# Kernel optimization log

Hardware: AMD Instinct MI355X
Metric: run time of the kernel (lower is better)

## Reference

```python
import jax, jax.numpy as jnp
import numpy as np

HEADS = 8
DIM_HEAD = 64
EPS = 1e-5

def chan_norm(x, g, b):
    # LayerNorm over channel dim (axis=1), biased variance
    mean = jnp.mean(x, axis=1, keepdims=True)
    var = jnp.var(x, axis=1, keepdims=True)
    return (x - mean) / jnp.sqrt(var + EPS) * g + b

def l2norm(x):
    n = jnp.sqrt(jnp.sum(x * x, axis=1, keepdims=True))
    return x / jnp.maximum(n, 1e-12)

def fold_heads(x, b):
    # b (h c) H W -> (b h) c H W
    _, hc, H, W = x.shape
    return x.reshape(b, HEADS, DIM_HEAD, H, W).reshape(b * HEADS, DIM_HEAD, H, W)

def setup_inputs() -> dict:
    key = jax.random.key(0)
    ks = jax.random.split(key, 8)
    dim = 256
    inner = HEADS * DIM_HEAD  # 512
    b, Hq, Wq = 8, 96, 96
    Hc, Wc = 64, 64
    s = 1.0 / np.sqrt(dim)
    return {
        "query_source": jax.random.normal(ks[0], (b, dim, Hq, Wq), jnp.float32),
        "context": jax.random.normal(ks[1], (b, dim, Hc, Wc), jnp.float32),
        "qs_g": jnp.ones((1, dim, 1, 1), jnp.float32),
        "qs_b": jnp.zeros((1, dim, 1, 1), jnp.float32),
        "ctx_g": jnp.ones((1, dim, 1, 1), jnp.float32),
        "ctx_b": jnp.zeros((1, dim, 1, 1), jnp.float32),
        "out_g": jnp.ones((1, dim, 1, 1), jnp.float32),
        "out_b": jnp.zeros((1, dim, 1, 1), jnp.float32),
        "w_q": jax.random.normal(ks[2], (inner, dim), jnp.float32) * s,
        "w_kv": jax.random.normal(ks[3], (2 * inner, dim), jnp.float32) * s,
        "w_out": jax.random.normal(ks[4], (dim, inner), jnp.float32) * (1.0 / np.sqrt(inner)),
        "gamma": jnp.full((1,), 0.5, jnp.float32),
    }

def reference(query_source, context, qs_g, qs_b, ctx_g, ctx_b, out_g, out_b, w_q, w_kv, w_out, gamma):
    b, c, Hq, Wq = query_source.shape
    Hc, Wc = context.shape[2], context.shape[3]
    h_top_k = int(Hc ** 0.5)
    w_top_k = int(Wc ** 0.5)

    ctx = chan_norm(context, ctx_g, ctx_b)
    qs = chan_norm(query_source, qs_g, qs_b)

    kv = jnp.einsum('oc,bchw->bohw', w_kv, ctx)  # 1x1 conv, no bias
    k, v = jnp.split(kv, 2, axis=1)
    q = jnp.einsum('oc,bchw->bohw', w_q, qs)

    q = fold_heads(q, b); k = fold_heads(k, b); v = fold_heads(v, b)
    q = l2norm(q); k = l2norm(k)  # cosine-sim attention

    if h_top_k < Hc or w_top_k < Wc:
        k_abs = jnp.abs(k)
        q_probe = jnp.sum(q, axis=(2, 3))  # (bh, d)
        if h_top_k < Hc:
            score_r = jnp.einsum('bc,bch->bh', q_probe, jnp.sum(k_abs, axis=3))
            top_h = jax.lax.top_k(score_r, h_top_k)[1]  # (bh, kh)
            k = jnp.take_along_axis(k, top_h[:, None, :, None], axis=2)
            v = jnp.take_along_axis(v, top_h[:, None, :, None], axis=2)
        if w_top_k < Wc:
            score_c = jnp.einsum('bc,bcw->bw', q_probe, jnp.sum(k_abs, axis=2))
            top_w = jax.lax.top_k(score_c, w_top_k)[1]  # (bh, kw)
            k = jnp.take_along_axis(k, top_w[:, None, None, :], axis=3)
            v = jnp.take_along_axis(v, top_w[:, None, None, :], axis=3)

    # b d h w -> b (h w) d
    flat = lambda t: t.transpose(0, 2, 3, 1).reshape(t.shape[0], -1, t.shape[1])
    qf, kf, vf = flat(q), flat(k), flat(v)

    sim = jnp.einsum('bid,bjd->bij', qf, kf)
    attn = jax.nn.softmax(sim, axis=-1)
    out = jnp.einsum('bij,bjd->bid', attn, vf)  # (bh, Hq*Wq, d)

    out = out.reshape(b, HEADS, Hq, Wq, DIM_HEAD).transpose(0, 1, 4, 2, 3)
    out = out.reshape(b, HEADS * DIM_HEAD, Hq, Wq)
    out = jnp.einsum('oc,bchw->bohw', w_out, out)
    out = chan_norm(out, out_g, out_b)
    return gamma * out + query_source
```

## Files before the change

kernel.cpp:

```cpp
#include <hip/hip_runtime.h>
#include <math.h>


#define EPSN 1e-5f

typedef __attribute__((ext_vector_type(8))) short bf16x8;
typedef __attribute__((ext_vector_type(4))) float f32x4;

__device__ inline unsigned short f2bf(float f) {
    unsigned u = __float_as_uint(f);
    u += 0x7fff + ((u >> 16) & 1);
    return (unsigned short)(u >> 16);
}
__device__ inline float bf2f(unsigned short h) {
    return __uint_as_float((unsigned)h << 16);
}

#define GL2LDS(g, s) __builtin_amdgcn_global_load_lds( \
    (const __attribute__((address_space(1))) void*)(g), \
    (__attribute__((address_space(3))) void*)(s), 16, 0, 0)

__global__ __launch_bounds__(256) void cvt_split_kernel(
    const float* __restrict__ x, unsigned short* __restrict__ hi,
    unsigned short* __restrict__ lo, int n)
{
    int i = blockIdx.x * 256 + threadIdx.x;
    if (i < n) {
        float v = x[i];
        unsigned short h = f2bf(v);
        hi[i] = h;
        lo[i] = f2bf(v - bf2f(h));
    }
}
__global__ __launch_bounds__(256) void cvt_bf16_kernel(
    const float* __restrict__ x, unsigned short* __restrict__ y, int n)
{
    int i = blockIdx.x * 256 + threadIdx.x;
    if (i < n) y[i] = f2bf(x[i]);
}

__global__ __launch_bounds__(256) void chan_norm_split_kernel(
    const float* __restrict__ x, const float* __restrict__ g,
    const float* __restrict__ bb, unsigned short* __restrict__ yh,
    unsigned short* __restrict__ yl, int N)
{
    int idx = blockIdx.x * 256 + threadIdx.x;
    int b = idx / N, p = idx - b * N;
    const float* xb = x + (size_t)b * 256 * N + p;
    float mean = 0.f, m2 = 0.f;
    for (int c = 0; c < 256; ++c) {
        float v = xb[(size_t)c * N];
        mean += v; m2 += v * v;
    }
    mean *= (1.f / 256.f); m2 *= (1.f / 256.f);
    float inv = 1.f / sqrtf(m2 - mean * mean + EPSN);
    uint4* yhr = (uint4*)(yh + ((size_t)b * N + p) * 256);
    uint4* ylr = (uint4*)(yl + ((size_t)b * N + p) * 256);
    for (int c0 = 0; c0 < 256; c0 += 8) {
        unsigned short hh[8], ll[8];
        #pragma unroll
        for (int j = 0; j < 8; ++j) {
            int c = c0 + j;
            float v = (xb[(size_t)c * N] - mean) * inv * g[c] + bb[c];
            hh[j] = f2bf(v);
            ll[j] = f2bf(v - bf2f(hh[j]));
        }
        uint4 ph, pl;
        ph.x = (unsigned)hh[0] | ((unsigned)hh[1] << 16);
        ph.y = (unsigned)hh[2] | ((unsigned)hh[3] << 16);
        ph.z = (unsigned)hh[4] | ((unsigned)hh[5] << 16);
        ph.w = (unsigned)hh[6] | ((unsigned)hh[7] << 16);
        pl.x = (unsigned)ll[0] | ((unsigned)ll[1] << 16);
        pl.y = (unsigned)ll[2] | ((unsigned)ll[3] << 16);
        pl.z = (unsigned)ll[4] | ((unsigned)ll[5] << 16);
        pl.w = (unsigned)ll[6] | ((unsigned)ll[7] << 16);
        yhr[c0 >> 3] = ph;
        ylr[c0 >> 3] = pl;
    }
}

template <int MODE>
__global__ __launch_bounds__(256) void gemm_x3(
    const unsigned short* __restrict__ Ah, const unsigned short* __restrict__ Al,
    const unsigned short* __restrict__ Bth, const unsigned short* __restrict__ Btl,
    void* __restrict__ Cv, float* __restrict__ qprobe,
    int M, int N, int K, long long strideBt, long long strideC)
{
    __shared__ unsigned short AsH[128 * 32], AsL[128 * 32];
    __shared__ unsigned short BsH[128 * 32], BsL[128 * 32];
    const unsigned short* BzH = Bth + (size_t)blockIdx.z * strideBt;
    const unsigned short* BzL = Btl + (size_t)blockIdx.z * strideBt;
    int n0 = blockIdx.x * 128, m0 = blockIdx.y * 128;
    int t = threadIdx.x;
    int w = t >> 6, l = t & 63;
    int wm = (w >> 1) * 64, wn = (w & 1) * 64;
    int lc = l & 15, quad = l >> 4;

    f32x4 acc[4][4];
    #pragma unroll
    for (int i = 0; i < 4; ++i)
        #pragma unroll
        for (int j = 0; j < 4; ++j) acc[i][j] = {0.f, 0.f, 0.f, 0.f};

    int srow = t >> 2;
    int sseg = (t & 3) * 8;
    for (int k0 = 0; k0 < K; k0 += 32) {
        size_t a0 = (size_t)(m0 + srow) * K + k0 + sseg;
        size_t a1 = (size_t)(m0 + 64 + srow) * K + k0 + sseg;
        size_t b0 = (size_t)(n0 + srow) * K + k0 + sseg;
        size_t b1 = (size_t)(n0 + 64 + srow) * K + k0 + sseg;
        __syncthreads();
        GL2LDS(Ah + a0, AsH + (size_t)t * 8);
        GL2LDS(Ah + a1, AsH + 2048 + (size_t)t * 8);
        GL2LDS(Al + a0, AsL + (size_t)t * 8);
        GL2LDS(Al + a1, AsL + 2048 + (size_t)t * 8);
        GL2LDS(BzH + b0, BsH + (size_t)t * 8);
        GL2LDS(BzH + b1, BsH + 2048 + (size_t)t * 8);
        GL2LDS(BzL + b0, BsL + (size_t)t * 8);
        GL2LDS(BzL + b1, BsL + 2048 + (size_t)t * 8);
        __syncthreads();
        bf16x8 ah[4], al_[4], bh_[4], bl_[4];
        #pragma unroll
        for (int i = 0; i < 4; ++i) {
            ah[i]  = *(const bf16x8*)(AsH + (size_t)(wm + i * 16 + lc) * 32 + quad * 8);
            al_[i] = *(const bf16x8*)(AsL + (size_t)(wm + i * 16 + lc) * 32 + quad * 8);
        }
        #pragma unroll
        for (int j = 0; j < 4; ++j) {
            bh_[j] = *(const bf16x8*)(BsH + (size_t)(wn + j * 16 + lc) * 32 + quad * 8);
            bl_[j] = *(const bf16x8*)(BsL + (size_t)(wn + j * 16 + lc) * 32 + quad * 8);
        }
        #pragma unroll
        for (int i = 0; i < 4; ++i)
            #pragma unroll
            for (int j = 0; j < 4; ++j) {
                acc[i][j] = __builtin_amdgcn_mfma_f32_16x16x32_bf16(al_[i], bh_[j], acc[i][j], 0, 0, 0);
                acc[i][j] = __builtin_amdgcn_mfma_f32_16x16x32_bf16(ah[i],  bl_[j], acc[i][j], 0, 0, 0);
                acc[i][j] = __builtin_amdgcn_mfma_f32_16x16x32_bf16(ah[i],  bh_[j], acc[i][j], 0, 0, 0);
            }
    }
    if (MODE == 0) {
        float* C = (float*)Cv;
        size_t cbase = (size_t)blockIdx.z * strideC;
        #pragma unroll
        for (int i = 0; i < 4; ++i)
            #pragma unroll
            for (int j = 0; j < 4; ++j)
                #pragma unroll
                for (int r = 0; r < 4; ++r) {
                    int row = m0 + wm + i * 16 + quad * 4 + r;
                    int col = n0 + wn + j * 16 + lc;
                    C[cbase + (size_t)row * N + col] = acc[i][j][r];
                }
    } else {
        float inv[4];
        #pragma unroll
        for (int j = 0; j < 4; ++j) {
            float s = 0.f;
            #pragma unroll
            for (int i = 0; i < 4; ++i)
                #pragma unroll
                for (int r = 0; r < 4; ++r) s += acc[i][j][r] * acc[i][j][r];
            s += __shfl_xor(s, 16);
            s += __shfl_xor(s, 32);
            inv[j] = 1.f / fmaxf(sqrtf(s), 1e-12f);
        }
        unsigned short* qbf = (unsigned short*)Cv;
        #pragma unroll
        for (int i = 0; i < 4; ++i) {
            int row0 = m0 + wm + i * 16 + quad * 4;
            int h = row0 >> 6, d0 = row0 & 63;
            #pragma unroll
            for (int j = 0; j < 4; ++j) {
                int col = n0 + wn + j * 16 + lc;
                size_t addr = ((size_t)(blockIdx.z * 8 + h) * 9216 + col) * 64 + d0;
                unsigned lo = (unsigned)f2bf(acc[i][j][0] * inv[j])
                            | ((unsigned)f2bf(acc[i][j][1] * inv[j]) << 16);
                unsigned hi = (unsigned)f2bf(acc[i][j][2] * inv[j])
                            | ((unsigned)f2bf(acc[i][j][3] * inv[j]) << 16);
                uint2 pk; pk.x = lo; pk.y = hi;
                *(uint2*)(qbf + addr) = pk;
            }
        }
        int bh = blockIdx.z * 8 + ((m0 + wm) >> 6);
        #pragma unroll
        for (int i = 0; i < 4; ++i)
            #pragma unroll
            for (int r = 0; r < 4; ++r) {
                float s = 0.f;
                #pragma unroll
                for (int j = 0; j < 4; ++j) s += acc[i][j][r] * inv[j];
                s += __shfl_xor(s, 1);
                s += __shfl_xor(s, 2);
                s += __shfl_xor(s, 4);
                s += __shfl_xor(s, 8);
                if (lc == 0)
                    atomicAdd(&qprobe[bh * 64 + i * 16 + quad * 4 + r], s);
            }
    }
}

__global__ __launch_bounds__(256) void gemm_mfma(
    const unsigned short* __restrict__ A, const unsigned short* __restrict__ Bt,
    float* __restrict__ C, int M, int N, int K,
    long long strideBt, long long strideC)
{
    __shared__ unsigned short As[128 * 32];
    __shared__ unsigned short Bs[128 * 32];
    const unsigned short* Bz = Bt + (size_t)blockIdx.z * strideBt;
    int n0 = blockIdx.x * 128, m0 = blockIdx.y * 128;
    int t = threadIdx.x;
    int w = t >> 6, l = t & 63;
    int wm = (w >> 1) * 64, wn = (w & 1) * 64;
    int lc = l & 15, quad = l >> 4;
    f32x4 acc[4][4];
    #pragma unroll
    for (int i = 0; i < 4; ++i)
        #pragma unroll
        for (int j = 0; j < 4; ++j) acc[i][j] = {0.f, 0.f, 0.f, 0.f};
    int srow = t >> 2, sseg = (t & 3) * 8;
    for (int k0 = 0; k0 < K; k0 += 32) {
        const unsigned short* ga0 = A  + (size_t)(m0 + srow)      * K + k0 + sseg;
        const unsigned short* ga1 = A  + (size_t)(m0 + 64 + srow) * K + k0 + sseg;
        const unsigned short* gb0 = Bz + (size_t)(n0 + srow)      * K + k0 + sseg;
        const unsigned short* gb1 = Bz + (size_t)(n0 + 64 + srow) * K + k0 + sseg;
        __syncthreads();
        GL2LDS(ga0, As + (size_t)t * 8);
        GL2LDS(ga1, As + 2048 + (size_t)t * 8);
        GL2LDS(gb0, Bs + (size_t)t * 8);
        GL2LDS(gb1, Bs + 2048 + (size_t)t * 8);
        __syncthreads();
        bf16x8 af[4], bfr[4];
        #pragma unroll
        for (int i = 0; i < 4; ++i)
            af[i] = *(const bf16x8*)(As + (size_t)(wm + i * 16 + lc) * 32 + quad * 8);
        #pragma unroll
        for (int j = 0; j < 4; ++j)
            bfr[j] = *(const bf16x8*)(Bs + (size_t)(wn + j * 16 + lc) * 32 + quad * 8);
        #pragma unroll
        for (int i = 0; i < 4; ++i)
            #pragma unroll
            for (int j = 0; j < 4; ++j)
                acc[i][j] = __builtin_amdgcn_mfma_f32_16x16x32_bf16(af[i], bfr[j], acc[i][j], 0, 0, 0);
    }
    size_t cbase = (size_t)blockIdx.z * strideC;
    #pragma unroll
    for (int i = 0; i < 4; ++i)
        #pragma unroll
        for (int j = 0; j < 4; ++j)
            #pragma unroll
            for (int r = 0; r < 4; ++r) {
                int row = m0 + wm + i * 16 + quad * 4 + r;
                int col = n0 + wn + j * 16 + lc;
                C[cbase + (size_t)row * N + col] = acc[i][j][r];
            }
}

__global__ __launch_bounds__(256) void l2inv_f32_kernel(
    const float* __restrict__ x, float* __restrict__ inv, int N,
    long long strideB, long long strideH)
{
    int idx = blockIdx.x * 256 + threadIdx.x;
    int bh = idx / N, p = idx - bh * N;
    const float* base = x + (size_t)(bh >> 3) * strideB + (size_t)(bh & 7) * strideH + p;
    float ss = 0.f;
    #pragma unroll 8
    for (int d = 0; d < 64; ++d) { float v = base[(size_t)d * N]; ss += v * v; }
    inv[idx] = 1.f / fmaxf(sqrtf(ss), 1e-12f);
}

__global__ __launch_bounds__(256) void krowcol_kernel(
    const float* __restrict__ k, const float* __restrict__ invnk,
    float* __restrict__ krow, float* __restrict__ kcol)
{
    int bh = blockIdx.x, b = bh >> 3, h = bh & 7;
    int d0 = blockIdx.y * 8;
    const float* kbase = k + ((size_t)b * 512 + (size_t)h * 64) * 4096;
    __shared__ float inv_s[4096];
    __shared__ float tile[64 * 65];
    int t = threadIdx.x;
    for (int l = t; l < 4096; l += 256) inv_s[l] = invnk[(size_t)bh * 4096 + l];
    for (int dd = 0; dd < 8; ++dd) {
        int d = d0 + dd;
        __syncthreads();
        for (int l = t; l < 4096; l += 256)
            tile[(l >> 6) * 65 + (l & 63)] = kbase[(size_t)d * 4096 + l];
        __syncthreads();
        if (t < 64) {
            float s = 0.f;
            for (int ww = 0; ww < 64; ++ww) s += fabsf(tile[t * 65 + ww]) * inv_s[t * 64 + ww];
            krow[((size_t)bh * 64 + d) * 64 + t] = s;
        } else if (t < 128) {
            int ww = t - 64;
            float s = 0.f;
            for (int hh = 0; hh < 64; ++hh) s += fabsf(tile[hh * 65 + ww]) * inv_s[hh * 64 + ww];
            kcol[((size_t)bh * 64 + d) * 64 + ww] = s;
        }
    }
}

__global__ void topk_kernel(const float* __restrict__ qprobe,
                            const float* __restrict__ krow,
                            const float* __restrict__ kcol,
                            int* __restrict__ toph, int* __restrict__ topw)
{
    int bh = blockIdx.x, t = threadIdx.x;
    __shared__ float qp[64], sr[64], sc[64];
    qp[t] = qprobe[bh * 64 + t];
    __syncthreads();
    float s1 = 0.f, s2 = 0.f;
    for (int d = 0; d < 64; ++d) {
        float qv = qp[d];
        s1 += qv * krow[((size_t)bh * 64 + d) * 64 + t];
        s2 += qv * kcol[((size_t)bh * 64 + d) * 64 + t];
    }
    sr[t] = s1; sc[t] = s2;
    __syncthreads();
    if (t == 0) {
        unsigned long long used = 0ull;
        for (int it = 0; it < 8; ++it) {
            int best = -1; float bv = -INFINITY;
            for (int i = 0; i < 64; ++i)
                if (!((used >> i) & 1ull) && sr[i] > bv) { bv = sr[i]; best = i; }
            if (best < 0) best = it;
            used |= 1ull << best;
            toph[bh * 8 + it] = best;
        }
        used = 0ull;
        for (int it = 0; it < 8; ++it) {
            int best = -1; float bv = -INFINITY;
            for (int i = 0; i < 64; ++i)
                if (!((used >> i) & 1ull) && sc[i] > bv) { bv = sc[i]; best = i; }
            if (best < 0) best = it;
            used |= 1ull << best;
            topw[bh * 8 + it] = best;
        }
    }
}

__global__ __launch_bounds__(256) void gather_k_kernel(
    const float* __restrict__ k, const float* __restrict__ invnk,
    const int* __restrict__ toph, const int* __restrict__ topw,
    unsigned short* __restrict__ ksel)
{
    int bh = blockIdx.x, b = bh >> 3, h = bh & 7;
    __shared__ int th_s[8], tw_s[8];
    if (threadIdx.x < 8) th_s[threadIdx.x] = toph[bh * 8 + threadIdx.x];
    else if (threadIdx.x < 16) tw_s[threadIdx.x - 8] = topw[bh * 8 + threadIdx.x - 8];
    __syncthreads();
    const float* kbase = k + ((size_t)b * 512 + (size_t)h * 64) * 4096;
    for (int l = threadIdx.x; l < 4096; l += 256) {
        int tok = l >> 6, d = l & 63;
        int p = th_s[tok >> 3] * 64 + tw_s[tok & 7];
        ksel[(size_t)bh * 4096 + l] = f2bf(kbase[(size_t)d * 4096 + p] * invnk[(size_t)bh * 4096 + p]);
    }
}

__global__ __launch_bounds__(256) void vsel_kernel(
    const float* __restrict__ w_kv, const unsigned short* __restrict__ ctxt,
    const int* __restrict__ toph, const int* __restrict__ topw,
    unsigned short* __restrict__ vt)
{
    int bh = blockIdx.x, b = bh >> 3, h = bh & 7;
    __shared__ int th_s[8], tw_s[8];
    if (threadIdx.x < 8) th_s[threadIdx.x] = toph[bh * 8 + threadIdx.x];
    else if (threadIdx.x < 16) tw_s[threadIdx.x - 8] = topw[bh * 8 + threadIdx.x - 8];
    __syncthreads();
    const unsigned short* cb = ctxt + (size_t)b * 4096 * 256;
    int l = blockIdx.y * 1024 + threadIdx.x;
    for (int it = 0; it < 4; ++it, l += 256) {
        int tok = l >> 6, d = l & 63;
        int p = th_s[tok >> 3] * 64 + tw_s[tok & 7];
        const float* wr = w_kv + (size_t)(512 + h * 64 + d) * 256;
        const unsigned short* cr = cb + (size_t)p * 256;
        float s = 0.f;
        for (int c = 0; c < 256; ++c) s += wr[c] * bf2f(cr[c]);
        vt[(size_t)bh * 4096 + d * 64 + tok] = f2bf(s);
    }
}

#define LPAD 72
__global__ __launch_bounds__(256) void attn_mfma_kernel(
    const unsigned short* __restrict__ q_pd, const unsigned short* __restrict__ ksel,
    const unsigned short* __restrict__ vt, unsigned short* __restrict__ attn_t)
{
    int bh = blockIdx.y, b = bh >> 3, h = bh & 7;
    __shared__ unsigned short Ks[64 * LPAD];
    __shared__ unsigned short Vs[64 * LPAD];
    __shared__ unsigned short Ps[4][16 * LPAD];
    int t = threadIdx.x, w = t >> 6, l = t & 63;
    int lc = l & 15, quad = l >> 4;
    {
        int r0 = t >> 3, c0 = (t & 7) * 8;
        const unsigned short* kg = ksel + (size_t)bh * 4096;
        const unsigned short* vg = vt + (size_t)bh * 4096;
        *(uint4*)(Ks + r0 * LPAD + c0)        = *(const uint4*)(kg + r0 * 64 + c0);
        *(uint4*)(Ks + (r0 + 32) * LPAD + c0) = *(const uint4*)(kg + (r0 + 32) * 64 + c0);
        *(uint4*)(Vs + r0 * LPAD + c0)        = *(const uint4*)(vg + r0 * 64 + c0);
        *(uint4*)(Vs + (r0 + 32) * LPAD + c0) = *(const uint4*)(vg + (r0 + 32) * 64 + c0);
    }
    __syncthreads();
    int p0 = blockIdx.x * 64 + w * 16;
    const unsigned short* qrow = q_pd + ((size_t)bh * 9216 + p0 + lc) * 64;
    bf16x8 aq0 = *(const bf16x8*)(qrow + quad * 8);
    bf16x8 aq1 = *(const bf16x8*)(qrow + 32 + quad * 8);
    f32x4 sacc[4];
    #pragma unroll
    for (int j = 0; j < 4; ++j) sacc[j] = {0.f, 0.f, 0.f, 0.f};
    #pragma unroll
    for (int j = 0; j < 4; ++j) {
        bf16x8 bk0 = *(const bf16x8*)(Ks + (j * 16 + lc) * LPAD + quad * 8);
        bf16x8 bk1 = *(const bf16x8*)(Ks + (j * 16 + lc) * LPAD + 32 + quad * 8);
        sacc[j] = __builtin_amdgcn_mfma_f32_16x16x32_bf16(aq0, bk0, sacc[j], 0, 0, 0);
        sacc[j] = __builtin_amdgcn_mfma_f32_16x16x32_bf16(aq1, bk1, sacc[j], 0, 0, 0);
    }
    float e[4][4], den[4] = {0.f, 0.f, 0.f, 0.f};
    #pragma unroll
    for (int j = 0; j < 4; ++j)
        #pragma unroll
        for (int r = 0; r < 4; ++r) {
            float v = __expf(sacc[j][r] - 1.f);
            e[j][r] = v; den[r] += v;
        }
    #pragma unroll
    for (int r = 0; r < 4; ++r) {
        den[r] += __shfl_xor(den[r], 1);
        den[r] += __shfl_xor(den[r], 2);
        den[r] += __shfl_xor(den[r], 4);
        den[r] += __shfl_xor(den[r], 8);
    }
    #pragma unroll
    for (int j = 0; j < 4; ++j)
        #pragma unroll
        for (int r = 0; r < 4; ++r)
            Ps[w][(quad * 4 + r) * LPAD + j * 16 + lc] = f2bf(e[j][r]);
    __syncthreads();
    bf16x8 ap0 = *(const bf16x8*)(Ps[w] + lc * LPAD + quad * 8);
    bf16x8 ap1 = *(const bf16x8*)(Ps[w] + lc * LPAD + 32 + quad * 8);
    f32x4 oacc[4];
    #pragma unroll
    for (int j = 0; j < 4; ++j) oacc[j] = {0.f, 0.f, 0.f, 0.f};
    #pragma unroll
    for (int j = 0; j < 4; ++j) {
        bf16x8 bv0 = *(const bf16x8*)(Vs + (j * 16 + lc) * LPAD + quad * 8);
        bf16x8 bv1 = *(const bf16x8*)(Vs + (j * 16 + lc) * LPAD + 32 + quad * 8);
        oacc[j] = __builtin_amdgcn_mfma_f32_16x16x32_bf16(ap0, bv0, oacc[j], 0, 0, 0);
        oacc[j] = __builtin_amdgcn_mfma_f32_16x16x32_bf16(ap1, bv1, oacc[j], 0, 0, 0);
    }
    float rd[4];
    #pragma unroll
    for (int r = 0; r < 4; ++r) rd[r] = 1.f / den[r];
    #pragma unroll
    for (int j = 0; j < 4; ++j)
        #pragma unroll
        for (int r = 0; r < 4; ++r) {
            int p = p0 + quad * 4 + r;
            int d = j * 16 + lc;
            attn_t[((size_t)b * 9216 + p) * 512 + h * 64 + d] = f2bf(oacc[j][r] * rd[r]);
        }
}

__global__ __launch_bounds__(256) void final_kernel(
    const float* __restrict__ g, const float* __restrict__ bb,
    const float* __restrict__ gamma, const float* __restrict__ qsrc,
    float* __restrict__ out)
{
    int idx = blockIdx.x * 256 + threadIdx.x;
    int b = idx / 9216, p = idx - b * 9216;
    float* xb = out + (size_t)b * 256 * 9216 + p;
    float mean = 0.f, m2 = 0.f;
    for (int c = 0; c < 256; ++c) {
        float v = xb[(size_t)c * 9216];
        mean += v; m2 += v * v;
    }
    mean *= (1.f / 256.f); m2 *= (1.f / 256.f);
    float inv = 1.f / sqrtf(m2 - mean * mean + EPSN);
    float gm = gamma[0];
    const float* qs = qsrc + (size_t)b * 256 * 9216 + p;
    for (int c = 0; c < 256; ++c) {
        float v = (xb[(size_t)c * 9216] - mean) * inv * g[c] + bb[c];
        xb[(size_t)c * 9216] = gm * v + qs[(size_t)c * 9216];
    }
}

extern "C" void kernel_launch(void* const* d_in, const int* in_sizes, int n_in,
                              void* d_out, int out_size, void* d_ws, size_t ws_size,
                              hipStream_t stream) {
    const float* qsrc  = (const float*)d_in[0];
    const float* ctx   = (const float*)d_in[1];
    const float* qs_g  = (const float*)d_in[2];
    const float* qs_b  = (const float*)d_in[3];
    const float* ctx_g = (const float*)d_in[4];
    const float* ctx_b = (const float*)d_in[5];
    const float* out_g = (const float*)d_in[6];
    const float* out_b = (const float*)d_in[7];
    const float* w_q   = (const float*)d_in[8];
    const float* w_kv  = (const float*)d_in[9];
    const float* w_out = (const float*)d_in[10];
    const float* gamma = (const float*)d_in[11];
    float* out = (float*)d_out;

    char* base = (char*)d_ws;
    unsigned short* qs_h  = (unsigned short*)(base + 0);
    unsigned short* qs_l  = (unsigned short*)(base + 37748736);
    float*          k_f   = (float*)        (base + 0);
    unsigned short* attn_t= (unsigned short*)(base + 0);
    unsigned short* q_pd  = (unsigned short*)(base + 75497472);
    unsigned short* ctx_h = (unsigned short*)(base + 150994944);
    unsigned short* ctx_l = (unsigned short*)(base + 167772160);
    char* S = base + 184549376;
    float* invnk = (float*)S;                     S += 262144 * 4;
    float* krow  = (float*)S;                     S += 262144 * 4;
    float* kcol  = (float*)S;                     S += 262144 * 4;
    float* qprob = (float*)S;                     S += 4096 * 4;
    unsigned short* ksel = (unsigned short*)S;    S += 262144 * 2;
    unsigned short* vt   = (unsigned short*)S;    S += 262144 * 2;
    int*   toph  = (int*)S;                       S += 512 * 4;
    int*   topw  = (int*)S;                       S += 512 * 4;
    unsigned short* wq_h = (unsigned short*)S;    S += 131072 * 2;
    unsigned short* wq_l = (unsigned short*)S;    S += 131072 * 2;
    unsigned short* wk_h = (unsigned short*)S;    S += 131072 * 2;
    unsigned short* wk_l = (unsigned short*)S;    S += 131072 * 2;
    unsigned short* wo_h = (unsigned short*)S;    S += 131072 * 2;

    cvt_split_kernel<<<512, 256, 0, stream>>>(w_q, wq_h, wq_l, 131072);
    cvt_split_kernel<<<512, 256, 0, stream>>>(w_kv, wk_h, wk_l, 131072);
    cvt_bf16_kernel<<<512, 256, 0, stream>>>(w_out, wo_h, 131072);
    hipMemsetAsync(qprob, 0, 4096 * sizeof(float), stream);
    chan_norm_split_kernel<<<288, 256, 0, stream>>>(qsrc, qs_g, qs_b, qs_h, qs_l, 9216);
    gemm_x3<1><<<dim3(72, 4, 8), 256, 0, stream>>>(
        wq_h, wq_l, qs_h, qs_l, q_pd, qprob, 512, 9216, 256,
        9216LL * 256, 0);
    chan_norm_split_kernel<<<128, 256, 0, stream>>>(ctx, ctx_g, ctx_b, ctx_h, ctx_l, 4096);
    gemm_x3<0><<<dim3(32, 4, 8), 256, 0, stream>>>(
        wk_h, wk_l, ctx_h, ctx_l, k_f, nullptr, 512, 4096, 256,
        4096LL * 256, 512LL * 4096);
    l2inv_f32_kernel<<<1024, 256, 0, stream>>>(k_f, invnk, 4096, 512LL * 4096, 64LL * 4096);
    krowcol_kernel<<<dim3(64, 8), 256, 0, stream>>>(k_f, invnk, krow, kcol);
    topk_kernel<<<64, 64, 0, stream>>>(qprob, krow, kcol, toph, topw);
    gather_k_kernel<<<64, 256, 0, stream>>>(k_f, invnk, toph, topw, ksel);
    vsel_kernel<<<dim3(64, 4), 256, 0, stream>>>(w_kv, ctx_h, toph, topw, vt);
    attn_mfma_kernel<<<dim3(144, 64), 256, 0, stream>>>(q_pd, ksel, vt, attn_t);
    gemm_mfma<<<dim3(72, 2, 8), 256, 0, stream>>>(
        wo_h, attn_t, out, 256, 9216, 512, 9216LL * 512, 256LL * 9216);
    final_kernel<<<288, 256, 0, stream>>>(out_g, out_b, gamma, qsrc, out);
}
```

Before: 790.3 us.

## Double-buffer LDS tiles in both MFMA GEMM kernels to overlap loads with compute

Both GEMM kernels now keep two LDS buffers per operand. The next K-slice is issued via global_load_lds while the current slice is consumed by MFMAs, which cuts one of the two barriers per iteration. The aim is to hide global-to-LDS latency behind matrix math. In exchange LDS use per block doubles (64KB for the split-precision kernel), which may lower occupancy. It also relies on the compiler's waitcnt placement before the barrier so the loads stay correct.

After: 793.6 us. Within noise of the previous version (+0.4%).

```diff
diff --git a/kernel.cpp b/kernel.cpp
--- a/kernel.cpp
+++ b/kernel.cpp
@@ -86,8 +86,8 @@
     void* __restrict__ Cv, float* __restrict__ qprobe,
     int M, int N, int K, long long strideBt, long long strideC)
 {
-    __shared__ unsigned short AsH[128 * 32], AsL[128 * 32];
-    __shared__ unsigned short BsH[128 * 32], BsL[128 * 32];
+    __shared__ unsigned short AsH[2][128 * 32], AsL[2][128 * 32];
+    __shared__ unsigned short BsH[2][128 * 32], BsL[2][128 * 32];
     const unsigned short* BzH = Bth + (size_t)blockIdx.z * strideBt;
     const unsigned short* BzL = Btl + (size_t)blockIdx.z * strideBt;
     int n0 = blockIdx.x * 128, m0 = blockIdx.y * 128;
@@ -104,31 +104,32 @@
 
     int srow = t >> 2;
     int sseg = (t & 3) * 8;
-    for (int k0 = 0; k0 < K; k0 += 32) {
+
+    auto stage = [&](int bi, int k0) {
         size_t a0 = (size_t)(m0 + srow) * K + k0 + sseg;
         size_t a1 = (size_t)(m0 + 64 + srow) * K + k0 + sseg;
         size_t b0 = (size_t)(n0 + srow) * K + k0 + sseg;
         size_t b1 = (size_t)(n0 + 64 + srow) * K + k0 + sseg;
-        __syncthreads();
-        GL2LDS(Ah + a0, AsH + (size_t)t * 8);
-        GL2LDS(Ah + a1, AsH + 2048 + (size_t)t * 8);
-        GL2LDS(Al + a0, AsL + (size_t)t * 8);
-        GL2LDS(Al + a1, AsL + 2048 + (size_t)t * 8);
-        GL2LDS(BzH + b0, BsH + (size_t)t * 8);
-        GL2LDS(BzH + b1, BsH + 2048 + (size_t)t * 8);
-        GL2LDS(BzL + b0, BsL + (size_t)t * 8);
-        GL2LDS(BzL + b1, BsL + 2048 + (size_t)t * 8);
-        __syncthreads();
+        GL2LDS(Ah + a0, &AsH[bi][(size_t)t * 8]);
+        GL2LDS(Ah + a1, &AsH[bi][2048 + (size_t)t * 8]);
+        GL2LDS(Al + a0, &AsL[bi][(size_t)t * 8]);
+        GL2LDS(Al + a1, &AsL[bi][2048 + (size_t)t * 8]);
+        GL2LDS(BzH + b0, &BsH[bi][(size_t)t * 8]);
+        GL2LDS(BzH + b1, &BsH[bi][2048 + (size_t)t * 8]);
+        GL2LDS(BzL + b0, &BsL[bi][(size_t)t * 8]);
+        GL2LDS(BzL + b1, &BsL[bi][2048 + (size_t)t * 8]);
+    };
+    auto compute = [&](int bi) {
         bf16x8 ah[4], al_[4], bh_[4], bl_[4];
         #pragma unroll
         for (int i = 0; i < 4; ++i) {
-            ah[i]  = *(const bf16x8*)(AsH + (size_t)(wm + i * 16 + lc) * 32 + quad * 8);
-            al_[i] = *(const bf16x8*)(AsL + (size_t)(wm + i * 16 + lc) * 32 + quad * 8);
+            ah[i]  = *(const bf16x8*)(&AsH[bi][(size_t)(wm + i * 16 + lc) * 32 + quad * 8]);
+            al_[i] = *(const bf16x8*)(&AsL[bi][(size_t)(wm + i * 16 + lc) * 32 + quad * 8]);
         }
         #pragma unroll
         for (int j = 0; j < 4; ++j) {
-            bh_[j] = *(const bf16x8*)(BsH + (size_t)(wn + j * 16 + lc) * 32 + quad * 8);
-            bl_[j] = *(const bf16x8*)(BsL + (size_t)(wn + j * 16 + lc) * 32 + quad * 8);
+            bh_[j] = *(const bf16x8*)(&BsH[bi][(size_t)(wn + j * 16 + lc) * 32 + quad * 8]);
+            bl_[j] = *(const bf16x8*)(&BsL[bi][(size_t)(wn + j * 16 + lc) * 32 + quad * 8]);
         }
         #pragma unroll
         for (int i = 0; i < 4; ++i)
@@ -138,7 +139,18 @@
                 acc[i][j] = __builtin_amdgcn_mfma_f32_16x16x32_bf16(ah[i],  bl_[j], acc[i][j], 0, 0, 0);
                 acc[i][j] = __builtin_amdgcn_mfma_f32_16x16x32_bf16(ah[i],  bh_[j], acc[i][j], 0, 0, 0);
             }
-    }
+    };
+
+    const int NS = K >> 5;
+    stage(0, 0);
+    __syncthreads();
+    for (int ks = 0; ks < NS - 1; ++ks) {
+        stage((ks + 1) & 1, (ks + 1) << 5);
+        compute(ks & 1);
+        __syncthreads();
+    }
+    compute((NS - 1) & 1);
+
     if (MODE == 0) {
         float* C = (float*)Cv;
         size_t cbase = (size_t)blockIdx.z * strideC;
@@ -205,8 +217,8 @@
     float* __restrict__ C, int M, int N, int K,
     long long strideBt, long long strideC)
 {
-    __shared__ unsigned short As[128 * 32];
-    __shared__ unsigned short Bs[128 * 32];
+    __shared__ unsigned short As[2][128 * 32];
+    __shared__ unsigned short Bs[2][128 * 32];
     const unsigned short* Bz = Bt + (size_t)blockIdx.z * strideBt;
     int n0 = blockIdx.x * 128, m0 = blockIdx.y * 128;
     int t = threadIdx.x;
@@ -219,30 +231,42 @@
         #pragma unroll
         for (int j = 0; j < 4; ++j) acc[i][j] = {0.f, 0.f, 0.f, 0.f};
     int srow = t >> 2, sseg = (t & 3) * 8;
-    for (int k0 = 0; k0 < K; k0 += 32) {
+
+    auto stage = [&](int bi, int k0) {
         const unsigned short* ga0 = A  + (size_t)(m0 + srow)      * K + k0 + sseg;
         const unsigned short* ga1 = A  + (size_t)(m0 + 64 + srow) * K + k0 + sseg;
         const unsigned short* gb0 = Bz + (size_t)(n0 + srow)      * K + k0 + sseg;
         const unsigned short* gb1 = Bz + (size_t)(n0 + 64 + srow) * K + k0 + sseg;
-        __syncthreads();
-        GL2LDS(ga0, As + (size_t)t * 8);
-        GL2LDS(ga1, As + 2048 + (size_t)t * 8);
-        GL2LDS(gb0, Bs + (size_t)t * 8);
-        GL2LDS(gb1, Bs + 2048 + (size_t)t * 8);
-        __syncthreads();
+        GL2LDS(ga0, &As[bi][(size_t)t * 8]);
+        GL2LDS(ga1, &As[bi][2048 + (size_t)t * 8]);
+        GL2LDS(gb0, &Bs[bi][(size_t)t * 8]);
+        GL2LDS(gb1, &Bs[bi][2048 + (size_t)t * 8]);
+    };
+    auto compute = [&](int bi) {
         bf16x8 af[4], bfr[4];
         #pragma unroll
         for (int i = 0; i < 4; ++i)
-            af[i] = *(const bf16x8*)(As + (size_t)(wm + i * 16 + lc) * 32 + quad * 8);
+            af[i] = *(const bf16x8*)(&As[bi][(size_t)(wm + i * 16 + lc) * 32 + quad * 8]);
         #pragma unroll
         for (int j = 0; j < 4; ++j)
-            bfr[j] = *(const bf16x8*)(Bs + (size_t)(wn + j * 16 + lc) * 32 + quad * 8);
+            bfr[j] = *(const bf16x8*)(&Bs[bi][(size_t)(wn + j * 16 + lc) * 32 + quad * 8]);
         #pragma unroll
         for (int i = 0; i < 4; ++i)
             #pragma unroll
             for (int j = 0; j < 4; ++j)
                 acc[i][j] = __builtin_amdgcn_mfma_f32_16x16x32_bf16(af[i], bfr[j], acc[i][j], 0, 0, 0);
-    }
+    };
+
+    const int NS = K >> 5;
+    stage(0, 0);
+    __syncthreads();
+    for (int ks = 0; ks < NS - 1; ++ks) {
+        stage((ks + 1) & 1, (ks + 1) << 5);
+        compute(ks & 1);
+        __syncthreads();
+    }
+    compute((NS - 1) & 1);
+
     size_t cbase = (size_t)blockIdx.z * strideC;
     #pragma unroll
     for (int i = 0; i < 4; ++i)
```

## Load GEMM MFMA fragments directly from global memory instead of LDS staging

Applied to the files above, without the earlier changes.

Both the split-bf16 GEMM and the plain bf16 GEMM stop staging A and B tiles in shared memory via global_load_lds. Each wave now loads its MFMA operand fragments straight from global memory, which removes both __syncthreads per K step and all LDS traffic. In exchange, data shared between waves of a block is fetched once per wave, roughly doubling global/L2 traffic. Each lane also reads 16-byte pieces from rows strided by K, so coalescing is worse than in the staged copy.

Result: slower. 924.1 us (+16.9%).

```diff
diff --git a/kernel.cpp b/kernel.cpp
--- a/kernel.cpp
+++ b/kernel.cpp
@@ -15,10 +15,6 @@
 __device__ inline float bf2f(unsigned short h) {
     return __uint_as_float((unsigned)h << 16);
 }
-
-#define GL2LDS(g, s) __builtin_amdgcn_global_load_lds( \
-    (const __attribute__((address_space(1))) void*)(g), \
-    (__attribute__((address_space(3))) void*)(s), 16, 0, 0)
 
 __global__ __launch_bounds__(256) void cvt_split_kernel(
     const float* __restrict__ x, unsigned short* __restrict__ hi,
@@ -86,8 +82,6 @@
     void* __restrict__ Cv, float* __restrict__ qprobe,
     int M, int N, int K, long long strideBt, long long strideC)
 {
-    __shared__ unsigned short AsH[128 * 32], AsL[128 * 32];
-    __shared__ unsigned short BsH[128 * 32], BsL[128 * 32];
     const unsigned short* BzH = Bth + (size_t)blockIdx.z * strideBt;
     const unsigned short* BzL = Btl + (size_t)blockIdx.z * strideBt;
     int n0 = blockIdx.x * 128, m0 = blockIdx.y * 128;
@@ -102,33 +96,21 @@
         #pragma unroll
         for (int j = 0; j < 4; ++j) acc[i][j] = {0.f, 0.f, 0.f, 0.f};
 
-    int srow = t >> 2;
-    int sseg = (t & 3) * 8;
+    const size_t astep = (size_t)16 * K;
+    size_t abase = (size_t)(m0 + wm + lc) * K + quad * 8;
+    size_t bbase = (size_t)(n0 + wn + lc) * K + quad * 8;
+
     for (int k0 = 0; k0 < K; k0 += 32) {
-        size_t a0 = (size_t)(m0 + srow) * K + k0 + sseg;
-        size_t a1 = (size_t)(m0 + 64 + srow) * K + k0 + sseg;
-        size_t b0 = (size_t)(n0 + srow) * K + k0 + sseg;
-        size_t b1 = (size_t)(n0 + 64 + srow) * K + k0 + sseg;
-        __syncthreads();
-        GL2LDS(Ah + a0, AsH + (size_t)t * 8);
-        GL2LDS(Ah + a1, AsH + 2048 + (size_t)t * 8);
-        GL2LDS(Al + a0, AsL + (size_t)t * 8);
-        GL2LDS(Al + a1, AsL + 2048 + (size_t)t * 8);
-        GL2LDS(BzH + b0, BsH + (size_t)t * 8);
-        GL2LDS(BzH + b1, BsH + 2048 + (size_t)t * 8);
-        GL2LDS(BzL + b0, BsL + (size_t)t * 8);
-        GL2LDS(BzL + b1, BsL + 2048 + (size_t)t * 8);
-        __syncthreads();
         bf16x8 ah[4], al_[4], bh_[4], bl_[4];
         #pragma unroll
         for (int i = 0; i < 4; ++i) {
-            ah[i]  = *(const bf16x8*)(AsH + (size_t)(wm + i * 16 + lc) * 32 + quad * 8);
-            al_[i] = *(const bf16x8*)(AsL + (size_t)(wm + i * 16 + lc) * 32 + quad * 8);
+            ah[i]  = *(const bf16x8*)(Ah + abase + (size_t)i * astep + k0);
+            al_[i] = *(const bf16x8*)(Al + abase + (size_t)i * astep + k0);
         }
         #pragma unroll
         for (int j = 0; j < 4; ++j) {
-            bh_[j] = *(const bf16x8*)(BsH + (size_t)(wn + j * 16 + lc) * 32 + quad * 8);
-            bl_[j] = *(const bf16x8*)(BsL + (size_t)(wn + j * 16 + lc) * 32 + quad * 8);
+            bh_[j] = *(const bf16x8*)(BzH + bbase + (size_t)j * astep + k0);
+            bl_[j] = *(const bf16x8*)(BzL + bbase + (size_t)j * astep + k0);
         }
         #pragma unroll
         for (int i = 0; i < 4; ++i)
@@ -139,6 +121,7 @@
                 acc[i][j] = __builtin_amdgcn_mfma_f32_16x16x32_bf16(ah[i],  bh_[j], acc[i][j], 0, 0, 0);
             }
     }
+
     if (MODE == 0) {
         float* C = (float*)Cv;
         size_t cbase = (size_t)blockIdx.z * strideC;
@@ -205,8 +188,6 @@
     float* __restrict__ C, int M, int N, int K,
     long long strideBt, long long strideC)
 {
-    __shared__ unsigned short As[128 * 32];
-    __shared__ unsigned short Bs[128 * 32];
     const unsigned short* Bz = Bt + (size_t)blockIdx.z * strideBt;
     int n0 = blockIdx.x * 128, m0 = blockIdx.y * 128;
     int t = threadIdx.x;
@@ -218,31 +199,26 @@
     for (int i = 0; i < 4; ++i)
         #pragma unroll
         for (int j = 0; j < 4; ++j) acc[i][j] = {0.f, 0.f, 0.f, 0.f};
-    int srow = t >> 2, sseg = (t & 3) * 8;
+
+    const size_t astep = (size_t)16 * K;
+    size_t abase = (size_t)(m0 + wm + lc) * K + quad * 8;
+    size_t bbase = (size_t)(n0 + wn + lc) * K + quad * 8;
+
     for (int k0 = 0; k0 < K; k0 += 32) {
-        const unsigned short* ga0 = A  + (size_t)(m0 + srow)      * K + k0 + sseg;
-        const unsigned short* ga1 = A  + (size_t)(m0 + 64 + srow) * K + k0 + sseg;
-        const unsigned short* gb0 = Bz + (size_t)(n0 + srow)      * K + k0 + sseg;
-        const unsigned short* gb1 = Bz + (size_t)(n0 + 64 + srow) * K + k0 + sseg;
-        __syncthreads();
-        GL2LDS(ga0, As + (size_t)t * 8);
-        GL2LDS(ga1, As + 2048 + (size_t)t * 8);
-        GL2LDS(gb0, Bs + (size_t)t * 8);
-        GL2LDS(gb1, Bs + 2048 + (size_t)t * 8);
-        __syncthreads();
         bf16x8 af[4], bfr[4];
         #pragma unroll
         for (int i = 0; i < 4; ++i)
-            af[i] = *(const bf16x8*)(As + (size_t)(wm + i * 16 + lc) * 32 + quad * 8);
+            af[i] = *(const bf16x8*)(A + abase + (size_t)i * astep + k0);
         #pragma unroll
         for (int j = 0; j < 4; ++j)
-            bfr[j] = *(const bf16x8*)(Bs + (size_t)(wn + j * 16 + lc) * 32 + quad * 8);
+            bfr[j] = *(const bf16x8*)(Bz + bbase + (size_t)j * astep + k0);
         #pragma unroll
         for (int i = 0; i < 4; ++i)
             #pragma unroll
             for (int j = 0; j < 4; ++j)
                 acc[i][j] = __builtin_amdgcn_mfma_f32_16x16x32_bf16(af[i], bfr[j], acc[i][j], 0, 0, 0);
     }
+
     size_t cbase = (size_t)blockIdx.z * strideC;
     #pragma unroll
     for (int i = 0; i < 4; ++i)
```

## Fuse output projection GEMM with channel LayerNorm and residual epilogue

Applied to the files above, without the earlier changes.

Replaces the separate output-projection GEMM and final channel-norm kernel with one kernel whose tile covers all 256 output channels for 64 pixels. Column mean and variance are reduced in registers and shared memory, then normalization, gamma scaling and the residual add are applied before the single write. This removes the write and two re-reads of the fp32 output tensor and one launch. In exchange the B tile shrinks to 64 columns, which lowers reuse of the loaded weights, and occupancy may change with the larger A tile in shared memory.

Result: faster. 720.2 us (-8.9%).

```diff
diff --git a/kernel.cpp b/kernel.cpp
--- a/kernel.cpp
+++ b/kernel.cpp
@@ -200,60 +200,105 @@
     }
 }
 
-__global__ __launch_bounds__(256) void gemm_mfma(
-    const unsigned short* __restrict__ A, const unsigned short* __restrict__ Bt,
-    float* __restrict__ C, int M, int N, int K,
-    long long strideBt, long long strideC)
-{
-    __shared__ unsigned short As[128 * 32];
-    __shared__ unsigned short Bs[128 * 32];
-    const unsigned short* Bz = Bt + (size_t)blockIdx.z * strideBt;
-    int n0 = blockIdx.x * 128, m0 = blockIdx.y * 128;
+__global__ __launch_bounds__(256) void gemm_out_fused(
+    const unsigned short* __restrict__ A,
+    const unsigned short* __restrict__ Bt,
+    const float* __restrict__ g, const float* __restrict__ bb,
+    const float* __restrict__ gamma, const float* __restrict__ qsrc,
+    float* __restrict__ out)
+{
+    __shared__ unsigned short As[256 * 32];
+    __shared__ unsigned short Bs[64 * 32];
+    __shared__ float2 colred[4][64];
+    int b = blockIdx.z;
+    const unsigned short* Bz = Bt + (size_t)b * 9216 * 512;
+    int n0 = blockIdx.x * 64;
     int t = threadIdx.x;
     int w = t >> 6, l = t & 63;
-    int wm = (w >> 1) * 64, wn = (w & 1) * 64;
     int lc = l & 15, quad = l >> 4;
+
     f32x4 acc[4][4];
     #pragma unroll
     for (int i = 0; i < 4; ++i)
         #pragma unroll
         for (int j = 0; j < 4; ++j) acc[i][j] = {0.f, 0.f, 0.f, 0.f};
+
     int srow = t >> 2, sseg = (t & 3) * 8;
-    for (int k0 = 0; k0 < K; k0 += 32) {
-        const unsigned short* ga0 = A  + (size_t)(m0 + srow)      * K + k0 + sseg;
-        const unsigned short* ga1 = A  + (size_t)(m0 + 64 + srow) * K + k0 + sseg;
-        const unsigned short* gb0 = Bz + (size_t)(n0 + srow)      * K + k0 + sseg;
-        const unsigned short* gb1 = Bz + (size_t)(n0 + 64 + srow) * K + k0 + sseg;
+    for (int k0 = 0; k0 < 512; k0 += 32) {
         __syncthreads();
-        GL2LDS(ga0, As + (size_t)t * 8);
-        GL2LDS(ga1, As + 2048 + (size_t)t * 8);
-        GL2LDS(gb0, Bs + (size_t)t * 8);
-        GL2LDS(gb1, Bs + 2048 + (size_t)t * 8);
+        #pragma unroll
+        for (int s = 0; s < 4; ++s)
+            GL2LDS(A + (size_t)(s * 64 + srow) * 512 + k0 + sseg,
+                   As + (size_t)s * 2048 + (size_t)t * 8);
+        GL2LDS(Bz + (size_t)(n0 + srow) * 512 + k0 + sseg, Bs + (size_t)t * 8);
         __syncthreads();
         bf16x8 af[4], bfr[4];
         #pragma unroll
         for (int i = 0; i < 4; ++i)
-            af[i] = *(const bf16x8*)(As + (size_t)(wm + i * 16 + lc) * 32 + quad * 8);
+            af[i] = *(const bf16x8*)(As + (size_t)(w * 64 + i * 16 + lc) * 32 + quad * 8);
         #pragma unroll
         for (int j = 0; j < 4; ++j)
-            bfr[j] = *(const bf16x8*)(Bs + (size_t)(wn + j * 16 + lc) * 32 + quad * 8);
+            bfr[j] = *(const bf16x8*)(Bs + (size_t)(j * 16 + lc) * 32 + quad * 8);
         #pragma unroll
         for (int i = 0; i < 4; ++i)
             #pragma unroll
             for (int j = 0; j < 4; ++j)
                 acc[i][j] = __builtin_amdgcn_mfma_f32_16x16x32_bf16(af[i], bfr[j], acc[i][j], 0, 0, 0);
     }
-    size_t cbase = (size_t)blockIdx.z * strideC;
+
+    float s_[4], ss_[4];
+    #pragma unroll
+    for (int j = 0; j < 4; ++j) {
+        float s = 0.f, ss = 0.f;
+        #pragma unroll
+        for (int i = 0; i < 4; ++i)
+            #pragma unroll
+            for (int r = 0; r < 4; ++r) {
+                float v = acc[i][j][r];
+                s += v; ss += v * v;
+            }
+        s  += __shfl_xor(s, 16);  s  += __shfl_xor(s, 32);
+        ss += __shfl_xor(ss, 16); ss += __shfl_xor(ss, 32);
+        s_[j] = s; ss_[j] = ss;
+    }
+    if (quad == 0) {
+        #pragma unroll
+        for (int j = 0; j < 4; ++j) {
+            colred[w][j * 16 + lc].x = s_[j];
+            colred[w][j * 16 + lc].y = ss_[j];
+        }
+    }
+    __syncthreads();
+    float mean[4], inv[4];
+    #pragma unroll
+    for (int j = 0; j < 4; ++j) {
+        float ts = 0.f, tss = 0.f;
+        #pragma unroll
+        for (int ww = 0; ww < 4; ++ww) {
+            float2 v = colred[ww][j * 16 + lc];
+            ts += v.x; tss += v.y;
+        }
+        float m = ts * (1.f / 256.f);
+        float var = tss * (1.f / 256.f) - m * m;
+        mean[j] = m;
+        inv[j] = 1.f / sqrtf(var + EPSN);
+    }
+    float gm = gamma[0];
+    const float* qsb = qsrc + (size_t)b * 256 * 9216;
+    float* ob = out + (size_t)b * 256 * 9216;
     #pragma unroll
     for (int i = 0; i < 4; ++i)
         #pragma unroll
-        for (int j = 0; j < 4; ++j)
-            #pragma unroll
-            for (int r = 0; r < 4; ++r) {
-                int row = m0 + wm + i * 16 + quad * 4 + r;
-                int col = n0 + wn + j * 16 + lc;
-                C[cbase + (size_t)row * N + col] = acc[i][j][r];
+        for (int r = 0; r < 4; ++r) {
+            int row = w * 64 + i * 16 + quad * 4 + r;
+            float gg = g[row], bv = bb[row];
+            #pragma unroll
+            for (int j = 0; j < 4; ++j) {
+                int col = n0 + j * 16 + lc;
+                float v = (acc[i][j][r] - mean[j]) * inv[j] * gg + bv;
+                ob[(size_t)row * 9216 + col] = gm * v + qsb[(size_t)row * 9216 + col];
             }
+        }
 }
 
 __global__ __launch_bounds__(256) void l2inv_f32_kernel(
@@ -460,29 +505,6 @@
         }
 }
 
-__global__ __launch_bounds__(256) void final_kernel(
-    const float* __restrict__ g, const float* __restrict__ bb,
-    const float* __restrict__ gamma, const float* __restrict__ qsrc,
-    float* __restrict__ out)
-{
-    int idx = blockIdx.x * 256 + threadIdx.x;
-    int b = idx / 9216, p = idx - b * 9216;
-    float* xb = out + (size_t)b * 256 * 9216 + p;
-    float mean = 0.f, m2 = 0.f;
-    for (int c = 0; c < 256; ++c) {
-        float v = xb[(size_t)c * 9216];
-        mean += v; m2 += v * v;
-    }
-    mean *= (1.f / 256.f); m2 *= (1.f / 256.f);
-    float inv = 1.f / sqrtf(m2 - mean * mean + EPSN);
-    float gm = gamma[0];
-    const float* qs = qsrc + (size_t)b * 256 * 9216 + p;
-    for (int c = 0; c < 256; ++c) {
-        float v = (xb[(size_t)c * 9216] - mean) * inv * g[c] + bb[c];
-        xb[(size_t)c * 9216] = gm * v + qs[(size_t)c * 9216];
-    }
-}
-
 extern "C" void kernel_launch(void* const* d_in, const int* in_sizes, int n_in,
                               void* d_out, int out_size, void* d_ws, size_t ws_size,
                               hipStream_t stream) {
@@ -541,7 +563,6 @@
     gather_k_kernel<<<64, 256, 0, stream>>>(k_f, invnk, toph, topw, ksel);
     vsel_kernel<<<dim3(64, 4), 256, 0, stream>>>(w_kv, ctx_h, toph, topw, vt);
     attn_mfma_kernel<<<dim3(144, 64), 256, 0, stream>>>(q_pd, ksel, vt, attn_t);
-    gemm_mfma<<<dim3(72, 2, 8), 256, 0, stream>>>(
-        wo_h, attn_t, out, 256, 9216, 512, 9216LL * 512, 256LL * 9216);
-    final_kernel<<<288, 256, 0, stream>>>(out_g, out_b, gamma, qsrc, out);
-}
+    gemm_out_fused<<<dim3(144, 1, 8), 256, 0, stream>>>(
+        wo_h, attn_t, out_g, out_b, gamma, qsrc, out);
+}
```
